# Performance work log

Hardware: AMD Instinct MI355X
Metric: run time of the kernel (lower is better)

## Reference

```python
import jax, jax.numpy as jnp
import numpy as np

D = 1536          # model dim
N = 12            # num heads
HD = D // N       # head dim = 128
C = HD // 2       # rope complex channels = 64
F, H, W = 4, 32, 32
L = F * H * W     # 4096 tokens
B = 1
S1 = C - 2 * (C // 3)   # 22 channels for the frame axis
S2 = C // 3             # 21 channels each for h and w axes
EPS = 1e-6


def setup_inputs() -> dict:
    key = jax.random.key(0)
    ks = jax.random.split(key, 9)
    sc = 1.0 / np.sqrt(D)
    inp = {"x": jax.random.normal(ks[0], (B, L, D), jnp.float32)}
    for i, name in enumerate(["wq", "wk", "wv", "wo"]):
        inp[name] = jax.random.normal(ks[1 + i], (D, D), jnp.float32) * sc
    for i, name in enumerate(["bq", "bk", "bv", "bo"]):
        inp[name] = jax.random.normal(ks[5 + i], (D,), jnp.float32) * 0.01
    inp["gq"] = jnp.ones((D,), jnp.float32)
    inp["gk"] = jnp.ones((D,), jnp.float32)
    # precomputed rotary tables: angle[pos, j] = pos * theta_j (complex freqs = cos + i sin)
    pos = jnp.arange(1024, dtype=jnp.float32)
    inv = 10000.0 ** (-jnp.arange(C, dtype=jnp.float32) / C)
    ang = pos[:, None] * inv[None, :]
    inp["freqs_cos"] = jnp.cos(ang)
    inp["freqs_sin"] = jnp.sin(ang)
    inp["seq_lens"] = jnp.full((B,), L, dtype=jnp.int32)
    inp["f_size"] = F
    inp["h_size"] = H
    inp["w_size"] = W
    return inp


def _rms(y, g):
    return y * jax.lax.rsqrt(jnp.mean(y * y, axis=-1, keepdims=True) + EPS) * g


def _grid(tab, f, h, w):
    # concat per-axis frequency bands: [f,h,w, S1 | S2 | rest] -> [L, 1, C]
    a = jnp.broadcast_to(tab[:f, None, None, :S1], (f, h, w, S1))
    b = jnp.broadcast_to(tab[None, :h, None, S1:S1 + S2], (f, h, w, S2))
    c = jnp.broadcast_to(tab[None, None, :w, S1 + S2:], (f, h, w, C - S1 - S2))
    return jnp.concatenate([a, b, c], axis=-1).reshape(f * h * w, 1, C)


def reference(x, wq, bq, wk, bk, wv, bv, wo, bo, gq, gk,
              freqs_cos, freqs_sin, seq_lens, f_size, h_size, w_size):
    b, l, dim = x.shape
    n = N
    d = dim // n
    c = d // 2
    # QKV projections with QK RMSNorm (norm over full model dim, as in the module)
    q = _rms(x @ wq.T + bq, gq).reshape(b, l, n, d)
    k = _rms(x @ wk.T + bk, gk).reshape(b, l, n, d)
    v = (x @ wv.T + bv).reshape(b, l, n, d)
    # 3D rotary: complex multiply by per-position grid frequencies
    cosg = _grid(freqs_cos, f_size, h_size, w_size)  # [L,1,C]
    sing = _grid(freqs_sin, f_size, h_size, w_size)

    def rope(t):
        tr = t.reshape(b, l, n, c, 2)
        xr, xi = tr[..., 0], tr[..., 1]
        return jnp.stack([xr * cosg - xi * sing, xr * sing + xi * cosg], axis=-1).reshape(b, l, n, d)

    q = rope(q)
    k = rope(k)
    # full (non-windowed) scaled dot-product attention, all k_lens == L
    scores = jnp.einsum('blnd,bmnd->bnlm', q, k) / jnp.sqrt(jnp.float32(d))
    attn = jax.nn.softmax(scores, axis=-1)
    out = jnp.einsum('bnlm,bmnd->blnd', attn, v).reshape(b, l, dim)
    return out @ wo.T + bo
```

## Files before the change

### kernel.cpp

```cpp
#include <hip/hip_runtime.h>
#include <math.h>

#define Dm   1536
#define NHd  12
#define HDm  128
#define Ltok 4096
#define S1c  22
#define S2c  21
#define MFIX 5.0f
#define LOG2E 1.4426950408889634f

typedef __attribute__((ext_vector_type(8))) _Float16 f16x8;
typedef __attribute__((ext_vector_type(4))) float f32x4;

static __device__ __forceinline__ f32x4 MFMA16(f16x8 a, f16x8 b, f32x4 c) {
  return __builtin_amdgcn_mfma_f32_16x16x32_f16(a, b, c, 0, 0, 0);
}

static __device__ __forceinline__ unsigned int pack_f16(float a, float b) {
  union { _Float16 h[2]; unsigned int u; } x;
  x.h[0] = (_Float16)a; x.h[1] = (_Float16)b;
  return x.u;
}

static __device__ __forceinline__ void gload_lds16(const void* g, void* l) {
  __builtin_amdgcn_global_load_lds(
      (const __attribute__((address_space(1))) unsigned int*)g,
      (__attribute__((address_space(3))) unsigned int*)l, 16, 0, 0);
}

__global__ __launch_bounds__(256) void cvt_f16(
    const float* __restrict__ src, unsigned short* __restrict__ dst, int nslots)
{
  int i = blockIdx.x * 256 + threadIdx.x;
  if (i >= nslots) return;
  float4 v = *(const float4*)&src[(size_t)i * 4];
  uint2 p;
  p.x = pack_f16(v.x, v.y);
  p.y = pack_f16(v.z, v.w);
  *(uint2*)&dst[(size_t)i * 4] = p;
}

__global__ __launch_bounds__(256) void cvt_w4_f16(
    const float* __restrict__ w0, const float* __restrict__ w1,
    const float* __restrict__ w2, const float* __restrict__ w3,
    unsigned short* __restrict__ dst)
{
  const int which = blockIdx.y;
  const float* src = (which == 0) ? w0 : (which == 1) ? w1 : (which == 2) ? w2 : w3;
  unsigned short* d = dst + (size_t)which * Dm * Dm;
  int i = blockIdx.x * 256 + threadIdx.x;
  float4 v = *(const float4*)&src[(size_t)i * 4];
  uint2 p;
  p.x = pack_f16(v.x, v.y);
  p.y = pack_f16(v.z, v.w);
  *(uint2*)&d[(size_t)i * 4] = p;
}

__global__ __launch_bounds__(256) void gemm_qkv_f16(
    const unsigned short* __restrict__ Ag, const unsigned short* __restrict__ Wg,
    const float* __restrict__ bq, const float* __restrict__ bk,
    const float* __restrict__ bv,
    float* __restrict__ qb, float* __restrict__ kb,
    unsigned short* __restrict__ vT)
{
  __shared__ __align__(16) unsigned short As[2][128][32], Bs[2][128][32];
  const int tid = threadIdx.x;
  const int w = tid >> 6, lane = tid & 63;
  const int nx = lane & 15, g = lane >> 4;
  const int m0 = blockIdx.y * 128, n0 = blockIdx.x * 128;
  const int wr = w >> 1, wc = w & 1;
  const int which = (n0 >= 2 * Dm) ? 2 : ((n0 >= Dm) ? 1 : 0);
  const int n0loc = n0 - which * Dm;

  const int srow = lane >> 2, scol = (lane & 3) * 8;
  const unsigned short* gp;
  char* lbase0;
  if (w < 2) {
    gp = Ag + (size_t)(m0 + w * 64 + srow) * Dm + scol;
    lbase0 = (char*)&As[0][0][0] + w * 4096;
  } else {
    gp = Wg + (size_t)(n0 + (w - 2) * 64 + srow) * Dm + scol;
    lbase0 = (char*)&Bs[0][0][0] + (w - 2) * 4096;
  }

  f32x4 acc[4][4];
#pragma unroll
  for (int i = 0; i < 4; i++)
#pragma unroll
    for (int j = 0; j < 4; j++) acc[i][j] = (f32x4){0.f, 0.f, 0.f, 0.f};

#pragma unroll
  for (int c = 0; c < 4; ++c)
    gload_lds16(gp + (size_t)c * 16 * Dm, lbase0 + c * 1024);
  gp += 32;
  __syncthreads();

  const int NK = Dm / 32;
  for (int it = 0; it < NK; ++it) {
    const int cur = it & 1;
    if (it + 1 < NK) {
      char* lb = lbase0 + (cur ^ 1) * 8192;
#pragma unroll
      for (int c = 0; c < 4; ++c)
        gload_lds16(gp + (size_t)c * 16 * Dm, lb + c * 1024);
      gp += 32;
    }
    f16x8 ah[4], bh[4];
#pragma unroll
    for (int i = 0; i < 4; ++i) {
      ah[i] = *(const f16x8*)&As[cur][wr * 64 + i * 16 + nx][g * 8];
      bh[i] = *(const f16x8*)&Bs[cur][wc * 64 + i * 16 + nx][g * 8];
    }
#pragma unroll
    for (int i = 0; i < 4; ++i)
#pragma unroll
      for (int j = 0; j < 4; ++j)
        acc[i][j] = MFMA16(ah[i], bh[j], acc[i][j]);
    __syncthreads();
  }

  if (which < 2) {
    float* Cout = which ? kb : qb;
    const float* bias = which ? bk : bq;
#pragma unroll
    for (int j = 0; j < 4; ++j) {
      const int col = n0loc + wc * 64 + j * 16 + nx;
      const float bz = bias[col];
#pragma unroll
      for (int i = 0; i < 4; ++i) {
        const int row0 = m0 + wr * 64 + i * 16 + g * 4;
#pragma unroll
        for (int r = 0; r < 4; ++r)
          Cout[(size_t)(row0 + r) * Dm + col] = acc[i][j][r] + bz;
      }
    }
  } else {
#pragma unroll
    for (int j = 0; j < 4; ++j) {
      const int col = n0loc + wc * 64 + j * 16 + nx;
      const float bz = bv[col];
#pragma unroll
      for (int i = 0; i < 4; ++i) {
        const int row0 = m0 + wr * 64 + i * 16 + g * 4;
        uint2 pk;
        pk.x = pack_f16(acc[i][j][0] + bz, acc[i][j][1] + bz);
        pk.y = pack_f16(acc[i][j][2] + bz, acc[i][j][3] + bz);
        *(uint2*)&vT[(size_t)col * Ltok + row0] = pk;
      }
    }
  }
}

__global__ __launch_bounds__(256) void gemm_nt_f16(
    const unsigned short* __restrict__ Ag, const unsigned short* __restrict__ Wg,
    const float* __restrict__ bias, float* __restrict__ Cout)
{
  __shared__ __align__(16) unsigned short As[2][128][32], Bs[2][128][32];
  const int tid = threadIdx.x;
  const int w = tid >> 6, lane = tid & 63;
  const int nx = lane & 15, g = lane >> 4;
  const int m0 = blockIdx.y * 128, n0 = blockIdx.x * 128;
  const int wr = w >> 1, wc = w & 1;

  const int srow = lane >> 2, scol = (lane & 3) * 8;
  const unsigned short* gp;
  char* lbase0;
  if (w < 2) {
    gp = Ag + (size_t)(m0 + w * 64 + srow) * Dm + scol;
    lbase0 = (char*)&As[0][0][0] + w * 4096;
  } else {
    gp = Wg + (size_t)(n0 + (w - 2) * 64 + srow) * Dm + scol;
    lbase0 = (char*)&Bs[0][0][0] + (w - 2) * 4096;
  }

  f32x4 acc[4][4];
#pragma unroll
  for (int i = 0; i < 4; i++)
#pragma unroll
    for (int j = 0; j < 4; j++) acc[i][j] = (f32x4){0.f, 0.f, 0.f, 0.f};

#pragma unroll
  for (int c = 0; c < 4; ++c)
    gload_lds16(gp + (size_t)c * 16 * Dm, lbase0 + c * 1024);
  gp += 32;
  __syncthreads();

  const int NK = Dm / 32;
  for (int it = 0; it < NK; ++it) {
    const int cur = it & 1;
    if (it + 1 < NK) {
      char* lb = lbase0 + (cur ^ 1) * 8192;
#pragma unroll
      for (int c = 0; c < 4; ++c)
        gload_lds16(gp + (size_t)c * 16 * Dm, lb + c * 1024);
      gp += 32;
    }
    f16x8 ah[4], bh[4];
#pragma unroll
    for (int i = 0; i < 4; ++i) {
      ah[i] = *(const f16x8*)&As[cur][wr * 64 + i * 16 + nx][g * 8];
      bh[i] = *(const f16x8*)&Bs[cur][wc * 64 + i * 16 + nx][g * 8];
    }
#pragma unroll
    for (int i = 0; i < 4; ++i)
#pragma unroll
      for (int j = 0; j < 4; ++j)
        acc[i][j] = MFMA16(ah[i], bh[j], acc[i][j]);
    __syncthreads();
  }
#pragma unroll
  for (int j = 0; j < 4; ++j) {
    const int col = n0 + wc * 64 + j * 16 + nx;
    const float bz = bias[col];
#pragma unroll
    for (int i = 0; i < 4; ++i) {
      const int row0 = m0 + wr * 64 + i * 16 + g * 4;
#pragma unroll
      for (int r = 0; r < 4; ++r)
        Cout[(size_t)(row0 + r) * Dm + col] = acc[i][j][r] + bz;
    }
  }
}

__global__ __launch_bounds__(256) void rmsnorm_rope_f16(
    float* __restrict__ q, float* __restrict__ k,
    const float* __restrict__ gq, const float* __restrict__ gk,
    const float* __restrict__ fcos, const float* __restrict__ fsin)
{
  const int l = blockIdx.x;
  const int tid = threadIdx.x;
  const int d0 = tid * 6;
  float qv[6], kv[6];
  float sq = 0.f, sk = 0.f;
  const float* qp = &q[(size_t)l * Dm + d0];
  const float* kp = &k[(size_t)l * Dm + d0];
#pragma unroll
  for (int i = 0; i < 6; i++) {
    qv[i] = qp[i]; sq += qv[i] * qv[i];
    kv[i] = kp[i]; sk += kv[i] * kv[i];
  }
#pragma unroll
  for (int s = 1; s < 64; s <<= 1) {
    sq += __shfl_xor(sq, s);
    sk += __shfl_xor(sk, s);
  }
  __shared__ float redq[4], redk[4];
  if ((tid & 63) == 0) { redq[tid >> 6] = sq; redk[tid >> 6] = sk; }
  __syncthreads();
  sq = redq[0] + redq[1] + redq[2] + redq[3];
  sk = redk[0] + redk[1] + redk[2] + redk[3];
  const float rq = rsqrtf(sq * (1.f / (float)Dm) + 1e-6f);
  const float rk = rsqrtf(sk * (1.f / (float)Dm) + 1e-6f);
  const float qscale = 0.08838834764831845f * LOG2E;
  const int f = l >> 10, h = (l >> 5) & 31, w = l & 31;
  unsigned short* qo = (unsigned short*)q + (size_t)l * Dm;
  unsigned short* ko = (unsigned short*)k + (size_t)l * Dm;
#pragma unroll
  for (int i = 0; i < 3; i++) {
    const int d = d0 + 2 * i;
    const int cc = (d & (HDm - 1)) >> 1;
    const int pos = (cc < S1c) ? f : ((cc < S1c + S2c) ? h : w);
    const float co = fcos[pos * 64 + cc];
    const float si = fsin[pos * 64 + cc];
    const float xr = qv[2 * i]     * rq * gq[d];
    const float xi = qv[2 * i + 1] * rq * gq[d + 1];
    *(unsigned int*)&qo[d] =
        pack_f16((xr * co - xi * si) * qscale, (xr * si + xi * co) * qscale);
    const float yr = kv[2 * i]     * rk * gk[d];
    const float yi = kv[2 * i + 1] * rk * gk[d + 1];
    *(unsigned int*)&ko[d] = pack_f16(yr * co - yi * si, yr * si + yi * co);
  }
}

__global__ __launch_bounds__(256, 3) void attn_f16(
    const unsigned short* __restrict__ qs, const unsigned short* __restrict__ ks,
    const unsigned short* __restrict__ vT,
    float* __restrict__ Op0, float* __restrict__ Op1,
    float* __restrict__ stats)
{
  __shared__ __align__(16) unsigned short Ks[2][32][136];
  __shared__ __align__(16) unsigned short Vs[2][128][40];
  __shared__ __align__(16) unsigned short Ps[4][32][40];

  const int tid = threadIdx.x;
  const int w = tid >> 6, lane = tid & 63;
  const int nx = lane & 15, g = lane >> 4;
  const int head = blockIdx.y;
  const int half = blockIdx.z;
  const int qbase = blockIdx.x * 128 + w * 32;
  const int kvbase = half * (Ltok / 2);
  float* __restrict__ Op = half ? Op1 : Op0;

  const float NEGMFIX2 = -MFIX * LOG2E;

  f16x8 vones;
#pragma unroll
  for (int i = 0; i < 8; i++) vones[i] = (_Float16)1.0f;

  f16x8 qf[2][4];
#pragma unroll
  for (int s = 0; s < 2; s++) {
    const unsigned short* qp =
        &qs[(size_t)(qbase + s * 16 + nx) * Dm + head * HDm + g * 8];
#pragma unroll
    for (int c = 0; c < 4; c++) qf[s][c] = *(const f16x8*)(qp + c * 32);
  }

  f32x4 oacc[2][9];
#pragma unroll
  for (int s = 0; s < 2; s++)
#pragma unroll
    for (int nt = 0; nt < 9; nt++) oacc[s][nt] = (f32x4){0.f, 0.f, 0.f, 0.f};

  const int krow = tid >> 3, kchb = (tid & 7) << 4;
  const int vrow = tid >> 1, vseg = (tid & 1) << 4;

  const unsigned short* kg = &ks[(size_t)(kvbase + krow) * Dm + head * HDm + kchb];
  const unsigned short* vg = &vT[((size_t)head * HDm + vrow) * Ltok + kvbase + vseg];

  {
    uint4 ka = *(const uint4*)kg, kb4 = *(const uint4*)(kg + 8);
    uint4 va = *(const uint4*)vg, vb4 = *(const uint4*)(vg + 8);
    *(uint4*)&Ks[0][krow][kchb]     = ka;
    *(uint4*)&Ks[0][krow][kchb + 8] = kb4;
    *(uint4*)&Vs[0][vrow][vseg]     = va;
    *(uint4*)&Vs[0][vrow][vseg + 8] = vb4;
  }
  __syncthreads();

  const int NIT = Ltok / 2 / 32;
  for (int t = 0; t < NIT; t++) {
    const int cur = t & 1, nxt = cur ^ 1;
    const bool pref = (t + 1 < NIT);
    uint4 ka, kb4, va, vb4;
    if (pref) {
      kg += 32 * Dm;
      vg += 32;
      ka  = *(const uint4*)kg;  kb4 = *(const uint4*)(kg + 8);
      va  = *(const uint4*)vg;  vb4 = *(const uint4*)(vg + 8);
    }

    f32x4 sa[2][2];
#pragma unroll
    for (int s = 0; s < 2; s++)
#pragma unroll
      for (int mt = 0; mt < 2; mt++)
        sa[s][mt] = (f32x4){NEGMFIX2, NEGMFIX2, NEGMFIX2, NEGMFIX2};
#pragma unroll
    for (int c = 0; c < 4; c++) {
      f16x8 k0f = *(const f16x8*)&Ks[cur][nx][c * 32 + g * 8];
      f16x8 k1f = *(const f16x8*)&Ks[cur][16 + nx][c * 32 + g * 8];
#pragma unroll
      for (int s = 0; s < 2; s++) {
        sa[s][0] = MFMA16(k0f, qf[s][c], sa[s][0]);
        sa[s][1] = MFMA16(k1f, qf[s][c], sa[s][1]);
      }
    }

#pragma unroll
    for (int s = 0; s < 2; s++) {
      float p[8];
#pragma unroll
      for (int r = 0; r < 4; r++) {
        p[r]     = __builtin_amdgcn_exp2f(sa[s][0][r]);
        p[4 + r] = __builtin_amdgcn_exp2f(sa[s][1][r]);
      }
#pragma unroll
      for (int mt = 0; mt < 2; mt++) {
        unsigned int u0 = pack_f16(p[4 * mt + 0], p[4 * mt + 1]);
        unsigned int u1 = pack_f16(p[4 * mt + 2], p[4 * mt + 3]);
        *(uint2*)&Ps[w][s * 16 + nx][mt * 16 + g * 4] = make_uint2(u0, u1);
      }
    }
    __builtin_amdgcn_sched_barrier(0);

    f16x8 ph[2];
#pragma unroll
    for (int s = 0; s < 2; s++)
      ph[s] = *(const f16x8*)&Ps[w][s * 16 + nx][g * 8];
#pragma unroll
    for (int nt = 0; nt < 8; nt++) {
      f16x8 vh = *(const f16x8*)&Vs[cur][nt * 16 + nx][g * 8];
#pragma unroll
      for (int s = 0; s < 2; s++)
        oacc[s][nt] = MFMA16(ph[s], vh, oacc[s][nt]);
    }
#pragma unroll
    for (int s = 0; s < 2; s++)
      oacc[s][8] = MFMA16(ph[s], vones, oacc[s][8]);

    if (pref) {
      *(uint4*)&Ks[nxt][krow][kchb]     = ka;
      *(uint4*)&Ks[nxt][krow][kchb + 8] = kb4;
      *(uint4*)&Vs[nxt][vrow][vseg]     = va;
      *(uint4*)&Vs[nxt][vrow][vseg + 8] = vb4;
    }
    __syncthreads();
  }

#pragma unroll
  for (int s = 0; s < 2; s++) {
#pragma unroll
    for (int nt = 0; nt < 8; nt++)
#pragma unroll
      for (int r = 0; r < 4; r++)
        Op[(size_t)(qbase + s * 16 + g * 4 + r) * Dm + head * HDm + nt * 16 + nx] =
            oacc[s][nt][r];
    if (nx == 0) {
#pragma unroll
      for (int r = 0; r < 4; r++)
        stats[((size_t)half * Ltok + qbase + s * 16 + g * 4 + r) * NHd + head] =
            oacc[s][8][r];
    }
  }
}

__global__ __launch_bounds__(384) void combine_f16(
    const float* __restrict__ Op0, const float* __restrict__ Op1,
    const float* __restrict__ stats, unsigned short* __restrict__ oh)
{
  const int row = blockIdx.x;
  const int c4 = threadIdx.x * 4;
  const int head = c4 >> 7;
  const float l0 = stats[(size_t)row * NHd + head];
  const float l1 = stats[((size_t)Ltok + row) * NHd + head];
  const float rl = 1.f / (l0 + l1);
  float4 o0 = *(const float4*)&Op0[(size_t)row * Dm + c4];
  float4 o1 = *(const float4*)&Op1[(size_t)row * Dm + c4];
  uint2 p;
  p.x = pack_f16((o0.x + o1.x) * rl, (o0.y + o1.y) * rl);
  p.y = pack_f16((o0.z + o1.z) * rl, (o0.w + o1.w) * rl);
  *(uint2*)&oh[(size_t)row * Dm + c4] = p;
}

extern "C" void kernel_launch(void* const* d_in, const int* in_sizes, int n_in,
                              void* d_out, int out_size, void* d_ws, size_t ws_size,
                              hipStream_t stream)
{
  const float* x    = (const float*)d_in[0];
  const float* wq   = (const float*)d_in[1];
  const float* wk   = (const float*)d_in[2];
  const float* wv   = (const float*)d_in[3];
  const float* wo   = (const float*)d_in[4];
  const float* bq   = (const float*)d_in[5];
  const float* bk   = (const float*)d_in[6];
  const float* bv   = (const float*)d_in[7];
  const float* bo   = (const float*)d_in[8];
  const float* gq   = (const float*)d_in[9];
  const float* gk   = (const float*)d_in[10];
  const float* fcos = (const float*)d_in[11];
  const float* fsin = (const float*)d_in[12];
  float* out = (float*)d_out;

  const size_t LD = (size_t)Ltok * Dm;
  const size_t WH = (size_t)Dm * Dm;
  float* base = (float*)d_ws;
  float* qb = base;
  float* kb = base + LD;
  unsigned short* vT  = (unsigned short*)(base + 2 * LD);
  unsigned short* xh  = (unsigned short*)(base + 2 * LD + LD / 2);
  float* Op0 = base + 2 * LD + LD / 2;
  float* Op1 = Op0 + LD;
  unsigned short* wqh = (unsigned short*)(Op1 + LD);
  unsigned short* woh = wqh + 3 * WH;
  unsigned short* oh  = (unsigned short*)base;
  float* stats = (float*)(wqh + 4 * WH);

  const int xslots = (int)(LD / 4);
  const int w4     = (int)(WH / 4);
  dim3 gqkv(3 * Dm / 128, Ltok / 128);
  dim3 gout(Dm / 128, Ltok / 128);

  cvt_f16<<<(xslots + 255) / 256, 256, 0, stream>>>(x, xh, xslots);
  cvt_w4_f16<<<dim3(w4 / 256, 4), 256, 0, stream>>>(wq, wk, wv, wo, wqh);

  gemm_qkv_f16<<<gqkv, 256, 0, stream>>>(xh, wqh, bq, bk, bv, qb, kb, vT);
  rmsnorm_rope_f16<<<Ltok, 256, 0, stream>>>(qb, kb, gq, gk, fcos, fsin);
  attn_f16<<<dim3(Ltok / 128, NHd, 2), 256, 0, stream>>>(
      (const unsigned short*)qb, (const unsigned short*)kb, vT, Op0, Op1, stats);
  combine_f16<<<Ltok, 384, 0, stream>>>(Op0, Op1, stats, oh);
  gemm_nt_f16<<<gout, 256, 0, stream>>>(oh, woh, bo, out);
}
```

Before: 409.6 us.

## Switch attention to 32x32 MFMA with register-resident P and explicit GEMM waitcnt

Rewrites the attention inner loop to use 32x32x16 MFMA, so each wave computes a 32-query by 32-key score tile and keeps P in registers via cross-half lane shuffles. This removes the per-wave LDS round trip for P and the extra ones-vector MFMA that produced row sums; the sums are now accumulated with scalar adds plus a shuffle. Separately, the GEMM loops replace __syncthreads with explicit vmcnt waits and raw s_barrier, letting the next tile's async LDS loads stay in flight across the barrier. The exchange is more shuffle and VALU work per tile, and the GEMM change depends on hand-counted outstanding loads being correct.

```diff
diff --git a/kernel.cpp b/kernel.cpp
--- a/kernel.cpp
+++ b/kernel.cpp
@@ -12,9 +12,13 @@
 
 typedef __attribute__((ext_vector_type(8))) _Float16 f16x8;
 typedef __attribute__((ext_vector_type(4))) float f32x4;
+typedef __attribute__((ext_vector_type(16))) float f32x16;
 
 static __device__ __forceinline__ f32x4 MFMA16(f16x8 a, f16x8 b, f32x4 c) {
   return __builtin_amdgcn_mfma_f32_16x16x32_f16(a, b, c, 0, 0, 0);
+}
+static __device__ __forceinline__ f32x16 MFMA32(f16x8 a, f16x8 b, f32x16 c) {
+  return __builtin_amdgcn_mfma_f32_32x32x16_f16(a, b, c, 0, 0, 0);
 }
 
 static __device__ __forceinline__ unsigned int pack_f16(float a, float b) {
@@ -94,7 +98,6 @@
   for (int c = 0; c < 4; ++c)
     gload_lds16(gp + (size_t)c * 16 * Dm, lbase0 + c * 1024);
   gp += 32;
-  __syncthreads();
 
   const int NK = Dm / 32;
   for (int it = 0; it < NK; ++it) {
@@ -105,7 +108,11 @@
       for (int c = 0; c < 4; ++c)
         gload_lds16(gp + (size_t)c * 16 * Dm, lb + c * 1024);
       gp += 32;
-    }
+      asm volatile("s_waitcnt vmcnt(4)" ::: "memory");
+    } else {
+      asm volatile("s_waitcnt vmcnt(0)" ::: "memory");
+    }
+    __builtin_amdgcn_s_barrier();
     f16x8 ah[4], bh[4];
 #pragma unroll
     for (int i = 0; i < 4; ++i) {
@@ -117,7 +124,7 @@
 #pragma unroll
       for (int j = 0; j < 4; ++j)
         acc[i][j] = MFMA16(ah[i], bh[j], acc[i][j]);
-    __syncthreads();
+    __builtin_amdgcn_s_barrier();
   }
 
   if (which < 2) {
@@ -184,7 +191,6 @@
   for (int c = 0; c < 4; ++c)
     gload_lds16(gp + (size_t)c * 16 * Dm, lbase0 + c * 1024);
   gp += 32;
-  __syncthreads();
 
   const int NK = Dm / 32;
   for (int it = 0; it < NK; ++it) {
@@ -195,7 +201,11 @@
       for (int c = 0; c < 4; ++c)
         gload_lds16(gp + (size_t)c * 16 * Dm, lb + c * 1024);
       gp += 32;
-    }
+      asm volatile("s_waitcnt vmcnt(4)" ::: "memory");
+    } else {
+      asm volatile("s_waitcnt vmcnt(0)" ::: "memory");
+    }
+    __builtin_amdgcn_s_barrier();
     f16x8 ah[4], bh[4];
 #pragma unroll
     for (int i = 0; i < 4; ++i) {
@@ -207,7 +217,7 @@
 #pragma unroll
       for (int j = 0; j < 4; ++j)
         acc[i][j] = MFMA16(ah[i], bh[j], acc[i][j]);
-    __syncthreads();
+    __builtin_amdgcn_s_barrier();
   }
 #pragma unroll
   for (int j = 0; j < 4; ++j) {
@@ -281,11 +291,10 @@
 {
   __shared__ __align__(16) unsigned short Ks[2][32][136];
   __shared__ __align__(16) unsigned short Vs[2][128][40];
-  __shared__ __align__(16) unsigned short Ps[4][32][40];
 
   const int tid = threadIdx.x;
   const int w = tid >> 6, lane = tid & 63;
-  const int nx = lane & 15, g = lane >> 4;
+  const int lx = lane & 31, hi = lane >> 5;
   const int head = blockIdx.y;
   const int half = blockIdx.z;
   const int qbase = blockIdx.x * 128 + w * 32;
@@ -294,24 +303,19 @@
 
   const float NEGMFIX2 = -MFIX * LOG2E;
 
-  f16x8 vones;
-#pragma unroll
-  for (int i = 0; i < 8; i++) vones[i] = (_Float16)1.0f;
-
-  f16x8 qf[2][4];
-#pragma unroll
-  for (int s = 0; s < 2; s++) {
-    const unsigned short* qp =
-        &qs[(size_t)(qbase + s * 16 + nx) * Dm + head * HDm + g * 8];
-#pragma unroll
-    for (int c = 0; c < 4; c++) qf[s][c] = *(const f16x8*)(qp + c * 32);
-  }
-
-  f32x4 oacc[2][9];
-#pragma unroll
-  for (int s = 0; s < 2; s++)
-#pragma unroll
-    for (int nt = 0; nt < 9; nt++) oacc[s][nt] = (f32x4){0.f, 0.f, 0.f, 0.f};
+  f16x8 qf[8];
+  {
+    const unsigned short* qp = &qs[(size_t)(qbase + lx) * Dm + head * HDm + hi * 8];
+#pragma unroll
+    for (int c = 0; c < 8; c++) qf[c] = *(const f16x8*)(qp + c * 16);
+  }
+
+  f32x16 oat[4];
+#pragma unroll
+  for (int nt = 0; nt < 4; nt++)
+#pragma unroll
+    for (int r = 0; r < 16; r++) oat[nt][r] = 0.f;
+  float lrow = 0.f;
 
   const int krow = tid >> 3, kchb = (tid & 7) << 4;
   const int vrow = tid >> 1, vseg = (tid & 1) << 4;
@@ -341,54 +345,51 @@
       va  = *(const uint4*)vg;  vb4 = *(const uint4*)(vg + 8);
     }
 
-    f32x4 sa[2][2];
-#pragma unroll
-    for (int s = 0; s < 2; s++)
-#pragma unroll
-      for (int mt = 0; mt < 2; mt++)
-        sa[s][mt] = (f32x4){NEGMFIX2, NEGMFIX2, NEGMFIX2, NEGMFIX2};
-#pragma unroll
-    for (int c = 0; c < 4; c++) {
-      f16x8 k0f = *(const f16x8*)&Ks[cur][nx][c * 32 + g * 8];
-      f16x8 k1f = *(const f16x8*)&Ks[cur][16 + nx][c * 32 + g * 8];
-#pragma unroll
-      for (int s = 0; s < 2; s++) {
-        sa[s][0] = MFMA16(k0f, qf[s][c], sa[s][0]);
-        sa[s][1] = MFMA16(k1f, qf[s][c], sa[s][1]);
-      }
-    }
-
-#pragma unroll
-    for (int s = 0; s < 2; s++) {
-      float p[8];
-#pragma unroll
-      for (int r = 0; r < 4; r++) {
-        p[r]     = __builtin_amdgcn_exp2f(sa[s][0][r]);
-        p[4 + r] = __builtin_amdgcn_exp2f(sa[s][1][r]);
-      }
-#pragma unroll
-      for (int mt = 0; mt < 2; mt++) {
-        unsigned int u0 = pack_f16(p[4 * mt + 0], p[4 * mt + 1]);
-        unsigned int u1 = pack_f16(p[4 * mt + 2], p[4 * mt + 3]);
-        *(uint2*)&Ps[w][s * 16 + nx][mt * 16 + g * 4] = make_uint2(u0, u1);
-      }
-    }
-    __builtin_amdgcn_sched_barrier(0);
-
-    f16x8 ph[2];
-#pragma unroll
-    for (int s = 0; s < 2; s++)
-      ph[s] = *(const f16x8*)&Ps[w][s * 16 + nx][g * 8];
-#pragma unroll
-    for (int nt = 0; nt < 8; nt++) {
-      f16x8 vh = *(const f16x8*)&Vs[cur][nt * 16 + nx][g * 8];
-#pragma unroll
-      for (int s = 0; s < 2; s++)
-        oacc[s][nt] = MFMA16(ph[s], vh, oacc[s][nt]);
-    }
-#pragma unroll
-    for (int s = 0; s < 2; s++)
-      oacc[s][8] = MFMA16(ph[s], vones, oacc[s][8]);
+    f32x16 sa;
+#pragma unroll
+    for (int r = 0; r < 16; r++) sa[r] = NEGMFIX2;
+#pragma unroll
+    for (int c = 0; c < 8; c++) {
+      f16x8 kf = *(const f16x8*)&Ks[cur][lx][c * 16 + hi * 8];
+      sa = MFMA32(kf, qf[c], sa);
+    }
+
+    float p[16], ps = 0.f;
+#pragma unroll
+    for (int r = 0; r < 16; r++) {
+      p[r] = __builtin_amdgcn_exp2f(sa[r]);
+      ps += p[r];
+    }
+    lrow += ps + __shfl_xor(ps, 32);
+
+    unsigned int W0 = pack_f16(p[0],  p[1]),  W1 = pack_f16(p[2],  p[3]);
+    unsigned int W2 = pack_f16(p[4],  p[5]),  W3 = pack_f16(p[6],  p[7]);
+    unsigned int W4 = pack_f16(p[8],  p[9]),  W5 = pack_f16(p[10], p[11]);
+    unsigned int W6 = pack_f16(p[12], p[13]), W7 = pack_f16(p[14], p[15]);
+
+#define HALFSWAP(Wa, Wb)                                            \
+    {                                                               \
+      unsigned int x_ = hi ? (Wa) : (Wb);                           \
+      unsigned int s_ = (unsigned int)__shfl_xor((int)x_, 32);      \
+      unsigned int na_ = hi ? s_ : (Wa);                            \
+      unsigned int nb_ = hi ? (Wb) : s_;                            \
+      (Wa) = na_; (Wb) = nb_;                                       \
+    }
+    HALFSWAP(W0, W2); HALFSWAP(W1, W3);
+    HALFSWAP(W4, W6); HALFSWAP(W5, W7);
+#undef HALFSWAP
+
+    union { unsigned int u[4]; f16x8 v; } pa0, pa1;
+    pa0.u[0] = W0; pa0.u[1] = W1; pa0.u[2] = W2; pa0.u[3] = W3;
+    pa1.u[0] = W4; pa1.u[1] = W5; pa1.u[2] = W6; pa1.u[3] = W7;
+
+#pragma unroll
+    for (int nt = 0; nt < 4; nt++) {
+      f16x8 v0 = *(const f16x8*)&Vs[cur][nt * 32 + lx][hi * 8];
+      f16x8 v1 = *(const f16x8*)&Vs[cur][nt * 32 + lx][16 + hi * 8];
+      oat[nt] = MFMA32(pa0.v, v0, oat[nt]);
+      oat[nt] = MFMA32(pa1.v, v1, oat[nt]);
+    }
 
     if (pref) {
       *(uint4*)&Ks[nxt][krow][kchb]     = ka;
@@ -400,20 +401,14 @@
   }
 
 #pragma unroll
-  for (int s = 0; s < 2; s++) {
-#pragma unroll
-    for (int nt = 0; nt < 8; nt++)
-#pragma unroll
-      for (int r = 0; r < 4; r++)
-        Op[(size_t)(qbase + s * 16 + g * 4 + r) * Dm + head * HDm + nt * 16 + nx] =
-            oacc[s][nt][r];
-    if (nx == 0) {
-#pragma unroll
-      for (int r = 0; r < 4; r++)
-        stats[((size_t)half * Ltok + qbase + s * 16 + g * 4 + r) * NHd + head] =
-            oacc[s][8][r];
-    }
-  }
+  for (int nt = 0; nt < 4; nt++)
+#pragma unroll
+    for (int r = 0; r < 16; r++) {
+      const int qo = (r & 3) + 8 * (r >> 2) + 4 * hi;
+      Op[(size_t)(qbase + qo) * Dm + head * HDm + nt * 32 + lx] = oat[nt][r];
+    }
+  if (hi == 0)
+    stats[((size_t)half * Ltok + qbase + lx) * NHd + head] = lrow;
 }
 
 __global__ __launch_bounds__(384) void combine_f16(
```

After: 414.9 us. About the same (+1.3%).
